# Performance work log

Measured on AMD Instinct MI355X. Metric: run time of the kernel, lower is better.

The kernel has to match this reference:

```python
import jax, jax.numpy as jnp
import numpy as np

N_NODES = 50000
N_EDGES = 800000
D = 64        # in_channels == out_channels
EDGE_DIM = 32
H = 8         # num_heads
HD = D // H   # head_dim


def _layer_norm(x, g, b, eps=1e-5):
    m = jnp.mean(x, axis=-1, keepdims=True)
    v = jnp.mean((x - m) ** 2, axis=-1, keepdims=True)
    return (x - m) * jax.lax.rsqrt(v + eps) * g + b


def setup_inputs() -> dict:
    key = jax.random.key(0)
    ks = jax.random.split(key, 20)
    s = 0.05
    inp = {
        'x': jax.random.normal(ks[0], (N_NODES, D), jnp.float32),
        'edge_index': jax.random.randint(ks[1], (2, N_EDGES), 0, N_NODES, dtype=jnp.int64),
        'edge_attr': jax.random.normal(ks[2], (N_EDGES, EDGE_DIM), jnp.float32),
        'Wq': jax.random.normal(ks[3], (D, D), jnp.float32) * s,
        'bq': jnp.zeros((D,), jnp.float32),
        'Wk': jax.random.normal(ks[4], (D, D), jnp.float32) * s,
        'bk': jnp.zeros((D,), jnp.float32),
        'Wv': jax.random.normal(ks[5], (D, D), jnp.float32) * s,
        'bv': jnp.zeros((D,), jnp.float32),
        'We': jax.random.normal(ks[6], (EDGE_DIM, D), jnp.float32) * s,
        'be': jnp.zeros((D,), jnp.float32),
        'Wo': jax.random.normal(ks[7], (D, D), jnp.float32) * s,
        'bo': jnp.zeros((D,), jnp.float32),
        'g1': jnp.ones((D,), jnp.float32),
        'b1': jnp.zeros((D,), jnp.float32),
        'g2': jnp.ones((D,), jnp.float32),
        'b2': jnp.zeros((D,), jnp.float32),
        'Wf1': jax.random.normal(ks[8], (D, 2 * D), jnp.float32) * s,
        'bf1': jnp.zeros((2 * D,), jnp.float32),
        'Wf2': jax.random.normal(ks[9], (2 * D, D), jnp.float32) * s,
        'bf2': jnp.zeros((D,), jnp.float32),
    }
    return inp


def reference(x, edge_index, edge_attr, Wq, bq, Wk, bk, Wv, bv, We, be, Wo, bo,
              g1, b1, g2, b2, Wf1, bf1, Wf2, bf2):
    num_nodes = x.shape[0]
    # add_self_loops with fill_value=0.0
    ar = jnp.arange(num_nodes, dtype=edge_index.dtype)
    src = jnp.concatenate([edge_index[0], ar])
    dst = jnp.concatenate([edge_index[1], ar])
    ea = jnp.concatenate([edge_attr, jnp.zeros((num_nodes, edge_attr.shape[1]), edge_attr.dtype)])

    q = (x @ Wq + bq).reshape(num_nodes, H, HD)
    k = (x @ Wk + bk).reshape(num_nodes, H, HD)
    v = (x @ Wv + bv).reshape(num_nodes, H, HD)
    ee = (ea @ We + be).reshape(-1, H, HD)  # [E', H, HD]

    # gather, score, global softmax over all edges (dim=0, as in source)
    scores = jnp.sum(q[dst] * (k[src] + ee), axis=-1) / (HD ** 0.5)  # [E', H]
    alpha = jax.nn.softmax(scores, axis=0)
    messages = alpha[..., None] * (v[src] + ee)  # [E', H, HD]

    out_sum = jax.ops.segment_sum(messages, dst, num_segments=num_nodes)
    counts = jax.ops.segment_sum(jnp.ones(dst.shape, x.dtype), dst, num_segments=num_nodes)
    counts = jnp.maximum(counts, 1.0)
    out = (out_sum / counts[:, None, None]).reshape(num_nodes, -1)

    h = _layer_norm(x + out @ Wo + bo, g1, b1)
    ffn = jax.nn.gelu(h @ Wf1 + bf1, approximate=False) @ Wf2 + bf2
    # dropout in eval mode -> identity
    return _layer_norm(h + ffn, g2, b2)
```

## Files before the change

### kernel.cpp

```cpp
#include <hip/hip_runtime.h>
#include <hip/hip_bf16.h>
#include <math.h>

#define N_NODES 50000
#define N_EDGES 800000
#define D 64
#define ED 32
#define NB 196

#define Q_OFF    0
#define KV8_OFF  1600000
#define EE_OFF   3200000
#define OS_OFF   16000000
#define S_OFF    17600000
#define RP_OFF   17600016
#define SRCP_OFF 17650018
#define POSE_OFF 18450018
#define DEG_OFF  19250018
#define WOFF_OFF 19300018
#define BSUM_OFF 19350018
#define H_OFF    0
#define F1_OFF   EE_OFF

typedef __bf16 bf16x8 __attribute__((ext_vector_type(8)));
typedef float  f32x4  __attribute__((ext_vector_type(4)));

__device__ __forceinline__ ushort f2bf(float f) {
  uint u = __float_as_uint(f);
  uint r = (u + 0x7FFFu + ((u >> 16) & 1u)) >> 16;
  return (ushort)r;
}
__device__ __forceinline__ float bfu2f(ushort u) {
  return __uint_as_float(((uint)u) << 16);
}
__device__ __forceinline__ void unpack8(uint4 u, float (&f)[8]) {
  f[0] = __uint_as_float(u.x << 16); f[1] = __uint_as_float(u.x & 0xffff0000u);
  f[2] = __uint_as_float(u.y << 16); f[3] = __uint_as_float(u.y & 0xffff0000u);
  f[4] = __uint_as_float(u.z << 16); f[5] = __uint_as_float(u.z & 0xffff0000u);
  f[6] = __uint_as_float(u.w << 16); f[7] = __uint_as_float(u.w & 0xffff0000u);
}
__device__ __forceinline__ void unfp8(uint2 u, float (&f)[8]) {
  f[0] = __builtin_amdgcn_cvt_f32_fp8((int)u.x, 0);
  f[1] = __builtin_amdgcn_cvt_f32_fp8((int)u.x, 1);
  f[2] = __builtin_amdgcn_cvt_f32_fp8((int)u.x, 2);
  f[3] = __builtin_amdgcn_cvt_f32_fp8((int)u.x, 3);
  f[4] = __builtin_amdgcn_cvt_f32_fp8((int)u.y, 0);
  f[5] = __builtin_amdgcn_cvt_f32_fp8((int)u.y, 1);
  f[6] = __builtin_amdgcn_cvt_f32_fp8((int)u.y, 2);
  f[7] = __builtin_amdgcn_cvt_f32_fp8((int)u.y, 3);
}
__device__ __forceinline__ bf16x8 pack_bf8(float4 a, float4 b) {
  bf16x8 r;
  r[0] = (__bf16)a.x; r[1] = (__bf16)a.y; r[2] = (__bf16)a.z; r[3] = (__bf16)a.w;
  r[4] = (__bf16)b.x; r[5] = (__bf16)b.y; r[6] = (__bf16)b.z; r[7] = (__bf16)b.w;
  return r;
}
__device__ __forceinline__ uint pk_fp8(f32x4 acc) {
  uint rr = (uint)__builtin_amdgcn_cvt_pk_fp8_f32(acc[0], acc[1], 0, false);
  return (uint)__builtin_amdgcn_cvt_pk_fp8_f32(acc[2], acc[3], (int)rr, true);
}

__global__ __launch_bounds__(256) void k_qkv_mfma(
    const float* __restrict__ x,
    const float* __restrict__ Wq, const float* __restrict__ bq,
    const float* __restrict__ Wk, const float* __restrict__ bk,
    const float* __restrict__ Wv, const float* __restrict__ bv,
    ushort* __restrict__ q, unsigned char* __restrict__ kv8,
    int* __restrict__ deg, float* __restrict__ S) {
  const int tid0 = blockIdx.x * 256 + threadIdx.x;
  if (tid0 < N_NODES) deg[tid0] = 0;
  if (tid0 < 16) S[tid0] = 0.f;

  const int lane = threadIdx.x & 63;
  const int wid  = threadIdx.x >> 6;
  const int r  = lane & 15;
  const int kg = lane >> 4;
  const float* Ws[3] = {Wq, Wk, Wv};
  const float* bs[3] = {bq, bk, bv};

  bf16x8 afrag[3][4][2];
  float  bias[3][4][4];
#pragma unroll
  for (int m = 0; m < 3; ++m)
#pragma unroll
    for (int nt = 0; nt < 4; ++nt) {
#pragma unroll
      for (int kk = 0; kk < 2; ++kk)
#pragma unroll
        for (int j = 0; j < 8; ++j)
          afrag[m][nt][kk][j] = (__bf16)Ws[m][(kk * 32 + kg * 8 + j) * 64 + nt * 16 + r];
#pragma unroll
      for (int j = 0; j < 4; ++j) bias[m][nt][j] = bs[m][nt * 16 + kg * 4 + j];
    }

  const int ntile = N_NODES / 16;
  const int nw = gridDim.x * 4;
  for (int t = blockIdx.x * 4 + wid; t < ntile; t += nw) {
    const int base = t * 16;
    const float4* xr = reinterpret_cast<const float4*>(x + (size_t)(base + r) * 64 + kg * 8);
    const bf16x8 xf0 = pack_bf8(xr[0], xr[1]);
    const bf16x8 xf1 = pack_bf8(xr[8], xr[9]);
#pragma unroll
    for (int m = 0; m < 3; ++m) {
#pragma unroll
      for (int nt = 0; nt < 4; ++nt) {
        f32x4 acc = {bias[m][nt][0], bias[m][nt][1], bias[m][nt][2], bias[m][nt][3]};
        acc = __builtin_amdgcn_mfma_f32_16x16x32_bf16(afrag[m][nt][0], xf0, acc, 0, 0, 0);
        acc = __builtin_amdgcn_mfma_f32_16x16x32_bf16(afrag[m][nt][1], xf1, acc, 0, 0, 0);
        if (m == 0) {
          ushort4 pk;
          pk.x = f2bf(acc[0]); pk.y = f2bf(acc[1]); pk.z = f2bf(acc[2]); pk.w = f2bf(acc[3]);
          *reinterpret_cast<ushort4*>(q + (size_t)(base + r) * 64 + nt * 16 + kg * 4) = pk;
        } else {
          const int sub = (m == 1) ? 0 : 8;
          const size_t off = (size_t)(base + r) * 128 +
                             (size_t)(nt * 2 + (kg >> 1)) * 16 + sub + (kg & 1) * 4;
          *reinterpret_cast<uint*>(kv8 + off) = pk_fp8(acc);
        }
      }
    }
  }
}

__global__ __launch_bounds__(256) void k_hist(const int* __restrict__ edst,
                                              int* __restrict__ deg) {
  const int i = blockIdx.x * 256 + threadIdx.x;
  if (i < N_EDGES) atomicAdd(&deg[edst[i]], 1);
}

__global__ __launch_bounds__(256) void k_scan_a(const int* __restrict__ deg,
                                                int* __restrict__ bsum) {
  __shared__ int lds[256];
  const int i = blockIdx.x * 256 + threadIdx.x;
  lds[threadIdx.x] = (i < N_NODES) ? deg[i] : 0;
  __syncthreads();
  for (int s = 128; s > 0; s >>= 1) {
    if (threadIdx.x < s) lds[threadIdx.x] += lds[threadIdx.x + s];
    __syncthreads();
  }
  if (threadIdx.x == 0) bsum[blockIdx.x] = lds[0];
}

__global__ __launch_bounds__(256) void k_scan_c(const int* __restrict__ deg,
                                                const int* __restrict__ bsum,
                                                int* __restrict__ rowptr,
                                                int* __restrict__ woff) {
  __shared__ int lds[256];
  const int t = threadIdx.x;
  lds[t] = (t < blockIdx.x) ? bsum[t] : 0;
  __syncthreads();
  for (int s = 128; s > 0; s >>= 1) {
    if (t < s) lds[t] += lds[t + s];
    __syncthreads();
  }
  const int base0 = lds[0];
  __syncthreads();
  const int i = blockIdx.x * 256 + t;
  const int d = (i < N_NODES) ? deg[i] : 0;
  lds[t] = d;
  __syncthreads();
  for (int off = 1; off < 256; off <<= 1) {
    const int val = (t >= off) ? lds[t - off] : 0;
    __syncthreads();
    lds[t] += val;
    __syncthreads();
  }
  const int ex = base0 + lds[t] - d;
  if (i < N_NODES) { rowptr[i] = ex; woff[i] = ex; }
  if (i == N_NODES - 1) rowptr[N_NODES] = ex + d;
}

__global__ __launch_bounds__(256) void k_scatter(const int* __restrict__ esrc,
                                                 const int* __restrict__ edst,
                                                 int* __restrict__ woff,
                                                 int* __restrict__ srcp,
                                                 int* __restrict__ pose) {
  const int i = blockIdx.x * 256 + threadIdx.x;
  if (i < N_EDGES) {
    const int pos = atomicAdd(&woff[edst[i]], 1);
    srcp[pos] = esrc[i];
    pose[i] = pos;
  }
}

__global__ __launch_bounds__(256) void k_ee_mfma(
    const int* __restrict__ pose, const float* __restrict__ ea,
    const float* __restrict__ We, const float* __restrict__ be,
    unsigned char* __restrict__ ee8) {
  const int lane = threadIdx.x & 63;
  const int wid  = threadIdx.x >> 6;
  const int r  = lane & 15;
  const int kg = lane >> 4;

  bf16x8 afrag[4];
  float  bias[4][4];
#pragma unroll
  for (int nt = 0; nt < 4; ++nt) {
#pragma unroll
    for (int j = 0; j < 8; ++j)
      afrag[nt][j] = (__bf16)We[(kg * 8 + j) * 64 + nt * 16 + r];
#pragma unroll
    for (int j = 0; j < 4; ++j) bias[nt][j] = be[nt * 16 + kg * 4 + j];
  }

  const int ntile = N_EDGES / 16;
  const int nw = gridDim.x * 4;
  for (int t = blockIdx.x * 4 + wid; t < ntile; t += nw) {
    const int base = t * 16;
    const int pos = pose[base + r];
    const float4* ar = reinterpret_cast<const float4*>(ea + (size_t)(base + r) * 32 + kg * 8);
    const bf16x8 bfrag = pack_bf8(ar[0], ar[1]);
#pragma unroll
    for (int nt = 0; nt < 4; ++nt) {
      f32x4 acc = {bias[nt][0], bias[nt][1], bias[nt][2], bias[nt][3]};
      acc = __builtin_amdgcn_mfma_f32_16x16x32_bf16(afrag[nt], bfrag, acc, 0, 0, 0);
      *reinterpret_cast<uint*>(ee8 + (size_t)pos * 64 + nt * 16 + kg * 4) = pk_fp8(acc);
    }
  }
}

__global__ __launch_bounds__(256) void k_gather(
    const int* __restrict__ rowptr, const int* __restrict__ srcp,
    const unsigned char* __restrict__ ee8,
    const ushort* __restrict__ qb, const unsigned char* __restrict__ kv8,
    const float* __restrict__ be,
    ushort* __restrict__ osum, float* __restrict__ S) {
  const int lane = threadIdx.x & 63;
  const int wid  = threadIdx.x >> 6;
  const int h = lane & 7, ei = lane >> 3;
  float bes[8];
#pragma unroll
  for (int i = 0; i < 8; ++i) bes[i] = be[h * 8 + i];
  float sacc = 0.f;
  const int nw = gridDim.x * 4;
  for (int n = blockIdx.x * 4 + wid; n < N_NODES; n += nw) {
    const int beg = rowptr[n], end = rowptr[n + 1];
    float qv[8];
    unpack8(*reinterpret_cast<const uint4*>(qb + (size_t)n * 64 + h * 8), qv);
    float macc[8];
#pragma unroll
    for (int i = 0; i < 8; ++i) macc[i] = 0.f;
    if (ei == 0) {
      float kv[8], vv[8];
      const uint4 kvl = *reinterpret_cast<const uint4*>(kv8 + (size_t)n * 128 + h * 16);
      unfp8(make_uint2(kvl.x, kvl.y), kv);
      unfp8(make_uint2(kvl.z, kvl.w), vv);
      float sc = 0.f;
#pragma unroll
      for (int i = 0; i < 8; ++i) sc = fmaf(qv[i], kv[i] + bes[i], sc);
      const float w = __expf(sc * 0.3535533905932738f);
      sacc += w;
#pragma unroll
      for (int i = 0; i < 8; ++i) macc[i] = w * (vv[i] + bes[i]);
    }
    int p = beg + ei;
    int src = (p < end) ? srcp[p] : 0;
    for (; p < end; p += 8) {
      const int nsrc = (p + 8 < end) ? srcp[p + 8] : 0;
      float ev[8], kv[8], vv[8];
      unfp8(*reinterpret_cast<const uint2*>(ee8 + (size_t)p * 64 + h * 8), ev);
      const uint4 kvl = *reinterpret_cast<const uint4*>(kv8 + (size_t)src * 128 + h * 16);
      unfp8(make_uint2(kvl.x, kvl.y), kv);
      unfp8(make_uint2(kvl.z, kvl.w), vv);
      float sc = 0.f;
#pragma unroll
      for (int i = 0; i < 8; ++i) sc = fmaf(qv[i], kv[i] + ev[i], sc);
      const float w = __expf(sc * 0.3535533905932738f);
      sacc += w;
#pragma unroll
      for (int i = 0; i < 8; ++i) macc[i] = fmaf(w, vv[i] + ev[i], macc[i]);
      src = nsrc;
    }
#pragma unroll
    for (int i = 0; i < 8; ++i) {
      macc[i] += __shfl_xor(macc[i], 8);
      macc[i] += __shfl_xor(macc[i], 16);
      macc[i] += __shfl_xor(macc[i], 32);
    }
    if (ei == 0) {
      uint pk[4];
#pragma unroll
      for (int i = 0; i < 4; ++i)
        pk[i] = (uint)f2bf(macc[2 * i]) | ((uint)f2bf(macc[2 * i + 1]) << 16);
      *reinterpret_cast<uint4*>(osum + (size_t)n * 64 + h * 8) =
          make_uint4(pk[0], pk[1], pk[2], pk[3]);
    }
  }
  sacc += __shfl_xor(sacc, 8);
  sacc += __shfl_xor(sacc, 16);
  sacc += __shfl_xor(sacc, 32);
  if (ei == 0) atomicAdd(&S[h], sacc);
}

__global__ __launch_bounds__(256) void k_ln1_mfma(
    const ushort* __restrict__ osum, const int* __restrict__ rowptr,
    const float* __restrict__ S, const float* __restrict__ x,
    const float* __restrict__ Wo, const float* __restrict__ bo,
    const float* __restrict__ g1, const float* __restrict__ b1,
    ushort* __restrict__ h) {
  const int lane = threadIdx.x & 63;
  const int wid  = threadIdx.x >> 6;
  const int r  = lane & 15;
  const int kg = lane >> 4;

  bf16x8 afrag[4][2];
  float bias[4][4], g1f[4][4], b1f[4][4];
#pragma unroll
  for (int nt = 0; nt < 4; ++nt) {
#pragma unroll
    for (int kk = 0; kk < 2; ++kk)
#pragma unroll
      for (int j = 0; j < 8; ++j)
        afrag[nt][kk][j] = (__bf16)Wo[(kk * 32 + kg * 8 + j) * 64 + nt * 16 + r];
#pragma unroll
    for (int j = 0; j < 4; ++j) {
      bias[nt][j] = bo[nt * 16 + kg * 4 + j];
      g1f[nt][j]  = g1[nt * 16 + kg * 4 + j];
      b1f[nt][j]  = b1[nt * 16 + kg * 4 + j];
    }
  }
  float invSv[8];
#pragma unroll
  for (int i = 0; i < 8; ++i) invSv[i] = 1.0f / S[i];

  const int ntile = N_NODES / 16;
  const int nw = gridDim.x * 4;
  for (int t = blockIdx.x * 4 + wid; t < ntile; t += nw) {
    const int node = t * 16 + r;
    const float invc = 1.0f / (float)(rowptr[node + 1] - rowptr[node] + 1);
    bf16x8 bfrag[2];
#pragma unroll
    for (int kk = 0; kk < 2; ++kk) {
      float tmp[8];
      unpack8(*reinterpret_cast<const uint4*>(osum + (size_t)node * 64 + kk * 32 + kg * 8), tmp);
      const float sc = invSv[kk * 4 + kg] * invc;
      bf16x8 bf;
#pragma unroll
      for (int e = 0; e < 8; ++e) bf[e] = (__bf16)(tmp[e] * sc);
      bfrag[kk] = bf;
    }
    float tv[4][4];
    float sum = 0.f;
#pragma unroll
    for (int nt = 0; nt < 4; ++nt) {
      f32x4 acc = {bias[nt][0], bias[nt][1], bias[nt][2], bias[nt][3]};
      acc = __builtin_amdgcn_mfma_f32_16x16x32_bf16(afrag[nt][0], bfrag[0], acc, 0, 0, 0);
      acc = __builtin_amdgcn_mfma_f32_16x16x32_bf16(afrag[nt][1], bfrag[1], acc, 0, 0, 0);
      const float4 xv = *reinterpret_cast<const float4*>(x + (size_t)node * 64 + nt * 16 + kg * 4);
      tv[nt][0] = acc[0] + xv.x; tv[nt][1] = acc[1] + xv.y;
      tv[nt][2] = acc[2] + xv.z; tv[nt][3] = acc[3] + xv.w;
      sum += (tv[nt][0] + tv[nt][1]) + (tv[nt][2] + tv[nt][3]);
    }
    sum += __shfl_xor(sum, 16);
    sum += __shfl_xor(sum, 32);
    const float m = sum * (1.0f / 64.0f);
    float var = 0.f;
#pragma unroll
    for (int nt = 0; nt < 4; ++nt)
#pragma unroll
      for (int j = 0; j < 4; ++j) { const float d = tv[nt][j] - m; var = fmaf(d, d, var); }
    var += __shfl_xor(var, 16);
    var += __shfl_xor(var, 32);
    const float rinv = rsqrtf(var * (1.0f / 64.0f) + 1e-5f);
#pragma unroll
    for (int nt = 0; nt < 4; ++nt) {
      ushort4 pk;
      pk.x = f2bf((tv[nt][0] - m) * rinv * g1f[nt][0] + b1f[nt][0]);
      pk.y = f2bf((tv[nt][1] - m) * rinv * g1f[nt][1] + b1f[nt][1]);
      pk.z = f2bf((tv[nt][2] - m) * rinv * g1f[nt][2] + b1f[nt][2]);
      pk.w = f2bf((tv[nt][3] - m) * rinv * g1f[nt][3] + b1f[nt][3]);
      *reinterpret_cast<ushort4*>(h + (size_t)node * 64 + nt * 16 + kg * 4) = pk;
    }
  }
}

__global__ __launch_bounds__(256) void k_ffn1_mfma(
    const ushort* __restrict__ h, const float* __restrict__ Wf1,
    const float* __restrict__ bf1, ushort* __restrict__ f1) {
  const int lane = threadIdx.x & 63;
  const int wid  = threadIdx.x >> 6;
  const int r  = lane & 15;
  const int kg = lane >> 4;

  bf16x8 afrag[8][2];
  float bias[8][4];
#pragma unroll
  for (int nt = 0; nt < 8; ++nt) {
#pragma unroll
    for (int kk = 0; kk < 2; ++kk)
#pragma unroll
      for (int j = 0; j < 8; ++j)
        afrag[nt][kk][j] = (__bf16)Wf1[(kk * 32 + kg * 8 + j) * 128 + nt * 16 + r];
#pragma unroll
    for (int j = 0; j < 4; ++j) bias[nt][j] = bf1[nt * 16 + kg * 4 + j];
  }

  const int ntile = N_NODES / 16;
  const int nw = gridDim.x * 4;
  for (int t = blockIdx.x * 4 + wid; t < ntile; t += nw) {
    const int node = t * 16 + r;
    const bf16x8 bf0 = *reinterpret_cast<const bf16x8*>(h + (size_t)node * 64 + kg * 8);
    const bf16x8 bf1g = *reinterpret_cast<const bf16x8*>(h + (size_t)node * 64 + 32 + kg * 8);
#pragma unroll
    for (int nt = 0; nt < 8; ++nt) {
      f32x4 acc = {bias[nt][0], bias[nt][1], bias[nt][2], bias[nt][3]};
      acc = __builtin_amdgcn_mfma_f32_16x16x32_bf16(afrag[nt][0], bf0, acc, 0, 0, 0);
      acc = __builtin_amdgcn_mfma_f32_16x16x32_bf16(afrag[nt][1], bf1g, acc, 0, 0, 0);
      ushort4 pk;
      pk.x = f2bf(0.5f * acc[0] * (1.0f + erff(acc[0] * 0.7071067811865475f)));
      pk.y = f2bf(0.5f * acc[1] * (1.0f + erff(acc[1] * 0.7071067811865475f)));
      pk.z = f2bf(0.5f * acc[2] * (1.0f + erff(acc[2] * 0.7071067811865475f)));
      pk.w = f2bf(0.5f * acc[3] * (1.0f + erff(acc[3] * 0.7071067811865475f)));
      *reinterpret_cast<ushort4*>(f1 + (size_t)node * 128 + nt * 16 + kg * 4) = pk;
    }
  }
}

__global__ __launch_bounds__(256) void k_ffn2_mfma(
    const ushort* __restrict__ f1, const ushort* __restrict__ h,
    const float* __restrict__ Wf2, const float* __restrict__ bf2,
    const float* __restrict__ g2, const float* __restrict__ b2,
    float* __restrict__ out) {
  const int lane = threadIdx.x & 63;
  const int wid  = threadIdx.x >> 6;
  const int r  = lane & 15;
  const int kg = lane >> 4;

  bf16x8 afrag[4][4];
  float bias[4][4], g2f[4][4], b2f[4][4];
#pragma unroll
  for (int nt = 0; nt < 4; ++nt) {
#pragma unroll
    for (int kk = 0; kk < 4; ++kk)
#pragma unroll
      for (int j = 0; j < 8; ++j)
        afrag[nt][kk][j] = (__bf16)Wf2[(kk * 32 + kg * 8 + j) * 64 + nt * 16 + r];
#pragma unroll
    for (int j = 0; j < 4; ++j) {
      bias[nt][j] = bf2[nt * 16 + kg * 4 + j];
      g2f[nt][j]  = g2[nt * 16 + kg * 4 + j];
      b2f[nt][j]  = b2[nt * 16 + kg * 4 + j];
    }
  }

  const int ntile = N_NODES / 16;
  const int nw = gridDim.x * 4;
  for (int t = blockIdx.x * 4 + wid; t < ntile; t += nw) {
    const int node = t * 16 + r;
    bf16x8 bfrag[4];
#pragma unroll
    for (int kk = 0; kk < 4; ++kk)
      bfrag[kk] = *reinterpret_cast<const bf16x8*>(f1 + (size_t)node * 128 + kk * 32 + kg * 8);
    float tv[4][4];
    float sum = 0.f;
#pragma unroll
    for (int nt = 0; nt < 4; ++nt) {
      f32x4 acc = {bias[nt][0], bias[nt][1], bias[nt][2], bias[nt][3]};
      acc = __builtin_amdgcn_mfma_f32_16x16x32_bf16(afrag[nt][0], bfrag[0], acc, 0, 0, 0);
      acc = __builtin_amdgcn_mfma_f32_16x16x32_bf16(afrag[nt][1], bfrag[1], acc, 0, 0, 0);
      acc = __builtin_amdgcn_mfma_f32_16x16x32_bf16(afrag[nt][2], bfrag[2], acc, 0, 0, 0);
      acc = __builtin_amdgcn_mfma_f32_16x16x32_bf16(afrag[nt][3], bfrag[3], acc, 0, 0, 0);
      const ushort4 hv = *reinterpret_cast<const ushort4*>(h + (size_t)node * 64 + nt * 16 + kg * 4);
      tv[nt][0] = acc[0] + bfu2f(hv.x); tv[nt][1] = acc[1] + bfu2f(hv.y);
      tv[nt][2] = acc[2] + bfu2f(hv.z); tv[nt][3] = acc[3] + bfu2f(hv.w);
      sum += (tv[nt][0] + tv[nt][1]) + (tv[nt][2] + tv[nt][3]);
    }
    sum += __shfl_xor(sum, 16);
    sum += __shfl_xor(sum, 32);
    const float m = sum * (1.0f / 64.0f);
    float var = 0.f;
#pragma unroll
    for (int nt = 0; nt < 4; ++nt)
#pragma unroll
      for (int j = 0; j < 4; ++j) { const float d = tv[nt][j] - m; var = fmaf(d, d, var); }
    var += __shfl_xor(var, 16);
    var += __shfl_xor(var, 32);
    const float rinv = rsqrtf(var * (1.0f / 64.0f) + 1e-5f);
#pragma unroll
    for (int nt = 0; nt < 4; ++nt) {
      float4 o;
      o.x = (tv[nt][0] - m) * rinv * g2f[nt][0] + b2f[nt][0];
      o.y = (tv[nt][1] - m) * rinv * g2f[nt][1] + b2f[nt][1];
      o.z = (tv[nt][2] - m) * rinv * g2f[nt][2] + b2f[nt][2];
      o.w = (tv[nt][3] - m) * rinv * g2f[nt][3] + b2f[nt][3];
      *reinterpret_cast<float4*>(out + (size_t)node * 64 + nt * 16 + kg * 4) = o;
    }
  }
}

extern "C" void kernel_launch(void* const* d_in, const int* in_sizes, int n_in,
                              void* d_out, int out_size, void* d_ws, size_t ws_size,
                              hipStream_t stream) {
  const float* x    = (const float*)d_in[0];
  const int*   ei   = (const int*)d_in[1];
  const int*   esrc = ei;
  const int*   edst = ei + N_EDGES;
  const float* ea   = (const float*)d_in[2];
  const float* Wq   = (const float*)d_in[3];
  const float* bq   = (const float*)d_in[4];
  const float* Wk   = (const float*)d_in[5];
  const float* bk   = (const float*)d_in[6];
  const float* Wv   = (const float*)d_in[7];
  const float* bv   = (const float*)d_in[8];
  const float* We   = (const float*)d_in[9];
  const float* be   = (const float*)d_in[10];
  const float* Wo   = (const float*)d_in[11];
  const float* bo   = (const float*)d_in[12];
  const float* g1   = (const float*)d_in[13];
  const float* b1   = (const float*)d_in[14];
  const float* g2   = (const float*)d_in[15];
  const float* b2   = (const float*)d_in[16];
  const float* Wf1  = (const float*)d_in[17];
  const float* bf1  = (const float*)d_in[18];
  const float* Wf2  = (const float*)d_in[19];
  const float* bf2  = (const float*)d_in[20];

  float* ws    = (float*)d_ws;
  ushort* q    = (ushort*)(ws + Q_OFF);
  unsigned char* kv8 = (unsigned char*)(ws + KV8_OFF);
  unsigned char* ee8 = (unsigned char*)(ws + EE_OFF);
  ushort* osum = (ushort*)(ws + OS_OFF);
  float* S     = ws + S_OFF;
  int*   rowptr = (int*)(ws + RP_OFF);
  int*   srcp   = (int*)(ws + SRCP_OFF);
  int*   pose   = (int*)(ws + POSE_OFF);
  int*   deg    = (int*)(ws + DEG_OFF);
  int*   woff   = (int*)(ws + WOFF_OFF);
  int*   bsum   = (int*)(ws + BSUM_OFF);
  ushort* h    = (ushort*)(ws + H_OFF);
  ushort* f1   = (ushort*)(ws + F1_OFF);
  float* out   = (float*)d_out;

  const dim3 B(256);
  const int edgeBlocks = (N_EDGES + 255) / 256;

  k_qkv_mfma<<<dim3(256), B, 0, stream>>>(x, Wq, bq, Wk, bk, Wv, bv, q, kv8, deg, S);
  k_hist<<<dim3(edgeBlocks), B, 0, stream>>>(edst, deg);
  k_scan_a<<<dim3(NB), B, 0, stream>>>(deg, bsum);
  k_scan_c<<<dim3(NB), B, 0, stream>>>(deg, bsum, rowptr, woff);
  k_scatter<<<dim3(edgeBlocks), B, 0, stream>>>(esrc, edst, woff, srcp, pose);
  k_ee_mfma<<<dim3(1024), B, 0, stream>>>(pose, ea, We, be, ee8);
  k_gather<<<dim3(1024), B, 0, stream>>>(rowptr, srcp, ee8, q, kv8, be, osum, S);
  k_ln1_mfma<<<dim3(256), B, 0, stream>>>(osum, rowptr, S, x, Wo, bo, g1, b1, h);
  k_ffn1_mfma<<<dim3(256), B, 0, stream>>>(h, Wf1, bf1, f1);
  k_ffn2_mfma<<<dim3(256), B, 0, stream>>>(f1, h, Wf2, bf2, g2, b2, out);
}
```

Measured before the change: 268.0 us.

## Fuse LN1, FFN1 and FFN2 into one post-attention kernel via LDS staging

Measured after the change: 264.2 us (median of 2 runs). About the same (-1.4%).

```diff
diff --git a/kernel.cpp b/kernel.cpp
--- a/kernel.cpp
+++ b/kernel.cpp
@@ -19,8 +19,6 @@
 #define DEG_OFF  19250018
 #define WOFF_OFF 19300018
 #define BSUM_OFF 19350018
-#define H_OFF    0
-#define F1_OFF   EE_OFF
 
 typedef __bf16 bf16x8 __attribute__((ext_vector_type(8)));
 typedef float  f32x4  __attribute__((ext_vector_type(4)));
@@ -292,32 +290,59 @@
   if (ei == 0) atomicAdd(&S[h], sacc);
 }
 
-__global__ __launch_bounds__(256) void k_ln1_mfma(
+#define HST 72
+#define FST 136
+__global__ __launch_bounds__(256, 1) void k_post(
     const ushort* __restrict__ osum, const int* __restrict__ rowptr,
     const float* __restrict__ S, const float* __restrict__ x,
     const float* __restrict__ Wo, const float* __restrict__ bo,
     const float* __restrict__ g1, const float* __restrict__ b1,
-    ushort* __restrict__ h) {
+    const float* __restrict__ Wf1, const float* __restrict__ bf1,
+    const float* __restrict__ Wf2, const float* __restrict__ bf2,
+    const float* __restrict__ g2, const float* __restrict__ b2,
+    float* __restrict__ out) {
+  __shared__ ushort hls[4][16 * HST];
+  __shared__ ushort f1ls[4][16 * FST];
   const int lane = threadIdx.x & 63;
   const int wid  = threadIdx.x >> 6;
   const int r  = lane & 15;
   const int kg = lane >> 4;
-
-  bf16x8 afrag[4][2];
-  float bias[4][4], g1f[4][4], b1f[4][4];
+  ushort* hbase  = &hls[wid][0];
+  ushort* f1base = &f1ls[wid][0];
+
+  bf16x8 wo[4][2], w1[8][2], w2[4][4];
+  float bof[4][4], g1f[4][4], b1f[4][4], b1v[8][4], bf2f[4][4], g2f[4][4], b2f[4][4];
 #pragma unroll
   for (int nt = 0; nt < 4; ++nt) {
 #pragma unroll
     for (int kk = 0; kk < 2; ++kk)
 #pragma unroll
       for (int j = 0; j < 8; ++j)
-        afrag[nt][kk][j] = (__bf16)Wo[(kk * 32 + kg * 8 + j) * 64 + nt * 16 + r];
+        wo[nt][kk][j] = (__bf16)Wo[(kk * 32 + kg * 8 + j) * 64 + nt * 16 + r];
+#pragma unroll
+    for (int kk = 0; kk < 4; ++kk)
+#pragma unroll
+      for (int j = 0; j < 8; ++j)
+        w2[nt][kk][j] = (__bf16)Wf2[(kk * 32 + kg * 8 + j) * 64 + nt * 16 + r];
 #pragma unroll
     for (int j = 0; j < 4; ++j) {
-      bias[nt][j] = bo[nt * 16 + kg * 4 + j];
-      g1f[nt][j]  = g1[nt * 16 + kg * 4 + j];
-      b1f[nt][j]  = b1[nt * 16 + kg * 4 + j];
-    }
+      bof[nt][j] = bo[nt * 16 + kg * 4 + j];
+      g1f[nt][j] = g1[nt * 16 + kg * 4 + j];
+      b1f[nt][j] = b1[nt * 16 + kg * 4 + j];
+      bf2f[nt][j] = bf2[nt * 16 + kg * 4 + j];
+      g2f[nt][j] = g2[nt * 16 + kg * 4 + j];
+      b2f[nt][j] = b2[nt * 16 + kg * 4 + j];
+    }
+  }
+#pragma unroll
+  for (int nt = 0; nt < 8; ++nt) {
+#pragma unroll
+    for (int kk = 0; kk < 2; ++kk)
+#pragma unroll
+      for (int j = 0; j < 8; ++j)
+        w1[nt][kk][j] = (__bf16)Wf1[(kk * 32 + kg * 8 + j) * 128 + nt * 16 + r];
+#pragma unroll
+    for (int j = 0; j < 4; ++j) b1v[nt][j] = bf1[nt * 16 + kg * 4 + j];
   }
   float invSv[8];
 #pragma unroll
@@ -343,9 +368,9 @@
     float sum = 0.f;
 #pragma unroll
     for (int nt = 0; nt < 4; ++nt) {
-      f32x4 acc = {bias[nt][0], bias[nt][1], bias[nt][2], bias[nt][3]};
-      acc = __builtin_amdgcn_mfma_f32_16x16x32_bf16(afrag[nt][0], bfrag[0], acc, 0, 0, 0);
-      acc = __builtin_amdgcn_mfma_f32_16x16x32_bf16(afrag[nt][1], bfrag[1], acc, 0, 0, 0);
+      f32x4 acc = {bof[nt][0], bof[nt][1], bof[nt][2], bof[nt][3]};
+      acc = __builtin_amdgcn_mfma_f32_16x16x32_bf16(wo[nt][0], bfrag[0], acc, 0, 0, 0);
+      acc = __builtin_amdgcn_mfma_f32_16x16x32_bf16(wo[nt][1], bfrag[1], acc, 0, 0, 0);
       const float4 xv = *reinterpret_cast<const float4*>(x + (size_t)node * 64 + nt * 16 + kg * 4);
       tv[nt][0] = acc[0] + xv.x; tv[nt][1] = acc[1] + xv.y;
       tv[nt][2] = acc[2] + xv.z; tv[nt][3] = acc[3] + xv.w;
@@ -362,127 +387,67 @@
     var += __shfl_xor(var, 16);
     var += __shfl_xor(var, 32);
     const float rinv = rsqrtf(var * (1.0f / 64.0f) + 1e-5f);
+    float hn[4][4];
 #pragma unroll
     for (int nt = 0; nt < 4; ++nt) {
+#pragma unroll
+      for (int j = 0; j < 4; ++j)
+        hn[nt][j] = (tv[nt][j] - m) * rinv * g1f[nt][j] + b1f[nt][j];
       ushort4 pk;
-      pk.x = f2bf((tv[nt][0] - m) * rinv * g1f[nt][0] + b1f[nt][0]);
-      pk.y = f2bf((tv[nt][1] - m) * rinv * g1f[nt][1] + b1f[nt][1]);
-      pk.z = f2bf((tv[nt][2] - m) * rinv * g1f[nt][2] + b1f[nt][2]);
-      pk.w = f2bf((tv[nt][3] - m) * rinv * g1f[nt][3] + b1f[nt][3]);
-      *reinterpret_cast<ushort4*>(h + (size_t)node * 64 + nt * 16 + kg * 4) = pk;
-    }
-  }
-}
-
-__global__ __launch_bounds__(256) void k_ffn1_mfma(
-    const ushort* __restrict__ h, const float* __restrict__ Wf1,
-    const float* __restrict__ bf1, ushort* __restrict__ f1) {
-  const int lane = threadIdx.x & 63;
-  const int wid  = threadIdx.x >> 6;
-  const int r  = lane & 15;
-  const int kg = lane >> 4;
-
-  bf16x8 afrag[8][2];
-  float bias[8][4];
-#pragma unroll
-  for (int nt = 0; nt < 8; ++nt) {
+      pk.x = f2bf(hn[nt][0]); pk.y = f2bf(hn[nt][1]);
+      pk.z = f2bf(hn[nt][2]); pk.w = f2bf(hn[nt][3]);
+      *reinterpret_cast<ushort4*>(hbase + r * HST + nt * 16 + kg * 4) = pk;
+    }
+    bf16x8 hB[2];
 #pragma unroll
     for (int kk = 0; kk < 2; ++kk)
-#pragma unroll
-      for (int j = 0; j < 8; ++j)
-        afrag[nt][kk][j] = (__bf16)Wf1[(kk * 32 + kg * 8 + j) * 128 + nt * 16 + r];
-#pragma unroll
-    for (int j = 0; j < 4; ++j) bias[nt][j] = bf1[nt * 16 + kg * 4 + j];
-  }
-
-  const int ntile = N_NODES / 16;
-  const int nw = gridDim.x * 4;
-  for (int t = blockIdx.x * 4 + wid; t < ntile; t += nw) {
-    const int node = t * 16 + r;
-    const bf16x8 bf0 = *reinterpret_cast<const bf16x8*>(h + (size_t)node * 64 + kg * 8);
-    const bf16x8 bf1g = *reinterpret_cast<const bf16x8*>(h + (size_t)node * 64 + 32 + kg * 8);
+      hB[kk] = *reinterpret_cast<const bf16x8*>(hbase + r * HST + kk * 32 + kg * 8);
 #pragma unroll
     for (int nt = 0; nt < 8; ++nt) {
-      f32x4 acc = {bias[nt][0], bias[nt][1], bias[nt][2], bias[nt][3]};
-      acc = __builtin_amdgcn_mfma_f32_16x16x32_bf16(afrag[nt][0], bf0, acc, 0, 0, 0);
-      acc = __builtin_amdgcn_mfma_f32_16x16x32_bf16(afrag[nt][1], bf1g, acc, 0, 0, 0);
+      f32x4 acc = {b1v[nt][0], b1v[nt][1], b1v[nt][2], b1v[nt][3]};
+      acc = __builtin_amdgcn_mfma_f32_16x16x32_bf16(w1[nt][0], hB[0], acc, 0, 0, 0);
+      acc = __builtin_amdgcn_mfma_f32_16x16x32_bf16(w1[nt][1], hB[1], acc, 0, 0, 0);
       ushort4 pk;
       pk.x = f2bf(0.5f * acc[0] * (1.0f + erff(acc[0] * 0.7071067811865475f)));
       pk.y = f2bf(0.5f * acc[1] * (1.0f + erff(acc[1] * 0.7071067811865475f)));
       pk.z = f2bf(0.5f * acc[2] * (1.0f + erff(acc[2] * 0.7071067811865475f)));
       pk.w = f2bf(0.5f * acc[3] * (1.0f + erff(acc[3] * 0.7071067811865475f)));
-      *reinterpret_cast<ushort4*>(f1 + (size_t)node * 128 + nt * 16 + kg * 4) = pk;
-    }
-  }
-}
-
-__global__ __launch_bounds__(256) void k_ffn2_mfma(
-    const ushort* __restrict__ f1, const ushort* __restrict__ h,
-    const float* __restrict__ Wf2, const float* __restrict__ bf2,
-    const float* __restrict__ g2, const float* __restrict__ b2,
-    float* __restrict__ out) {
-  const int lane = threadIdx.x & 63;
-  const int wid  = threadIdx.x >> 6;
-  const int r  = lane & 15;
-  const int kg = lane >> 4;
-
-  bf16x8 afrag[4][4];
-  float bias[4][4], g2f[4][4], b2f[4][4];
-#pragma unroll
-  for (int nt = 0; nt < 4; ++nt) {
+      *reinterpret_cast<ushort4*>(f1base + r * FST + nt * 16 + kg * 4) = pk;
+    }
+    bf16x8 fB[4];
 #pragma unroll
     for (int kk = 0; kk < 4; ++kk)
-#pragma unroll
-      for (int j = 0; j < 8; ++j)
-        afrag[nt][kk][j] = (__bf16)Wf2[(kk * 32 + kg * 8 + j) * 64 + nt * 16 + r];
-#pragma unroll
-    for (int j = 0; j < 4; ++j) {
-      bias[nt][j] = bf2[nt * 16 + kg * 4 + j];
-      g2f[nt][j]  = g2[nt * 16 + kg * 4 + j];
-      b2f[nt][j]  = b2[nt * 16 + kg * 4 + j];
-    }
-  }
-
-  const int ntile = N_NODES / 16;
-  const int nw = gridDim.x * 4;
-  for (int t = blockIdx.x * 4 + wid; t < ntile; t += nw) {
-    const int node = t * 16 + r;
-    bf16x8 bfrag[4];
-#pragma unroll
-    for (int kk = 0; kk < 4; ++kk)
-      bfrag[kk] = *reinterpret_cast<const bf16x8*>(f1 + (size_t)node * 128 + kk * 32 + kg * 8);
-    float tv[4][4];
-    float sum = 0.f;
+      fB[kk] = *reinterpret_cast<const bf16x8*>(f1base + r * FST + kk * 32 + kg * 8);
+    float sum2 = 0.f;
 #pragma unroll
     for (int nt = 0; nt < 4; ++nt) {
-      f32x4 acc = {bias[nt][0], bias[nt][1], bias[nt][2], bias[nt][3]};
-      acc = __builtin_amdgcn_mfma_f32_16x16x32_bf16(afrag[nt][0], bfrag[0], acc, 0, 0, 0);
-      acc = __builtin_amdgcn_mfma_f32_16x16x32_bf16(afrag[nt][1], bfrag[1], acc, 0, 0, 0);
-      acc = __builtin_amdgcn_mfma_f32_16x16x32_bf16(afrag[nt][2], bfrag[2], acc, 0, 0, 0);
-      acc = __builtin_amdgcn_mfma_f32_16x16x32_bf16(afrag[nt][3], bfrag[3], acc, 0, 0, 0);
-      const ushort4 hv = *reinterpret_cast<const ushort4*>(h + (size_t)node * 64 + nt * 16 + kg * 4);
-      tv[nt][0] = acc[0] + bfu2f(hv.x); tv[nt][1] = acc[1] + bfu2f(hv.y);
-      tv[nt][2] = acc[2] + bfu2f(hv.z); tv[nt][3] = acc[3] + bfu2f(hv.w);
-      sum += (tv[nt][0] + tv[nt][1]) + (tv[nt][2] + tv[nt][3]);
-    }
-    sum += __shfl_xor(sum, 16);
-    sum += __shfl_xor(sum, 32);
-    const float m = sum * (1.0f / 64.0f);
-    float var = 0.f;
+      f32x4 acc = {bf2f[nt][0], bf2f[nt][1], bf2f[nt][2], bf2f[nt][3]};
+      acc = __builtin_amdgcn_mfma_f32_16x16x32_bf16(w2[nt][0], fB[0], acc, 0, 0, 0);
+      acc = __builtin_amdgcn_mfma_f32_16x16x32_bf16(w2[nt][1], fB[1], acc, 0, 0, 0);
+      acc = __builtin_amdgcn_mfma_f32_16x16x32_bf16(w2[nt][2], fB[2], acc, 0, 0, 0);
+      acc = __builtin_amdgcn_mfma_f32_16x16x32_bf16(w2[nt][3], fB[3], acc, 0, 0, 0);
+      tv[nt][0] = acc[0] + hn[nt][0]; tv[nt][1] = acc[1] + hn[nt][1];
+      tv[nt][2] = acc[2] + hn[nt][2]; tv[nt][3] = acc[3] + hn[nt][3];
+      sum2 += (tv[nt][0] + tv[nt][1]) + (tv[nt][2] + tv[nt][3]);
+    }
+    sum2 += __shfl_xor(sum2, 16);
+    sum2 += __shfl_xor(sum2, 32);
+    const float m2 = sum2 * (1.0f / 64.0f);
+    float var2 = 0.f;
 #pragma unroll
     for (int nt = 0; nt < 4; ++nt)
 #pragma unroll
-      for (int j = 0; j < 4; ++j) { const float d = tv[nt][j] - m; var = fmaf(d, d, var); }
-    var += __shfl_xor(var, 16);
-    var += __shfl_xor(var, 32);
-    const float rinv = rsqrtf(var * (1.0f / 64.0f) + 1e-5f);
+      for (int j = 0; j < 4; ++j) { const float d = tv[nt][j] - m2; var2 = fmaf(d, d, var2); }
+    var2 += __shfl_xor(var2, 16);
+    var2 += __shfl_xor(var2, 32);
+    const float rinv2 = rsqrtf(var2 * (1.0f / 64.0f) + 1e-5f);
 #pragma unroll
     for (int nt = 0; nt < 4; ++nt) {
       float4 o;
-      o.x = (tv[nt][0] - m) * rinv * g2f[nt][0] + b2f[nt][0];
-      o.y = (tv[nt][1] - m) * rinv * g2f[nt][1] + b2f[nt][1];
-      o.z = (tv[nt][2] - m) * rinv * g2f[nt][2] + b2f[nt][2];
-      o.w = (tv[nt][3] - m) * rinv * g2f[nt][3] + b2f[nt][3];
+      o.x = (tv[nt][0] - m2) * rinv2 * g2f[nt][0] + b2f[nt][0];
+      o.y = (tv[nt][1] - m2) * rinv2 * g2f[nt][1] + b2f[nt][1];
+      o.z = (tv[nt][2] - m2) * rinv2 * g2f[nt][2] + b2f[nt][2];
+      o.w = (tv[nt][3] - m2) * rinv2 * g2f[nt][3] + b2f[nt][3];
       *reinterpret_cast<float4*>(out + (size_t)node * 64 + nt * 16 + kg * 4) = o;
     }
   }
@@ -527,8 +492,6 @@
   int*   deg    = (int*)(ws + DEG_OFF);
   int*   woff   = (int*)(ws + WOFF_OFF);
   int*   bsum   = (int*)(ws + BSUM_OFF);
-  ushort* h    = (ushort*)(ws + H_OFF);
-  ushort* f1   = (ushort*)(ws + F1_OFF);
   float* out   = (float*)d_out;
 
   const dim3 B(256);
@@ -541,7 +504,6 @@
   k_scatter<<<dim3(edgeBlocks), B, 0, stream>>>(esrc, edst, woff, srcp, pose);
   k_ee_mfma<<<dim3(1024), B, 0, stream>>>(pose, ea, We, be, ee8);
   k_gather<<<dim3(1024), B, 0, stream>>>(rowptr, srcp, ee8, q, kv8, be, osum, S);
-  k_ln1_mfma<<<dim3(256), B, 0, stream>>>(osum, rowptr, S, x, Wo, bo, g1, b1, h);
-  k_ffn1_mfma<<<dim3(256), B, 0, stream>>>(h, Wf1, bf1, f1);
-  k_ffn2_mfma<<<dim3(256), B, 0, stream>>>(f1, h, Wf2, bf2, g2, b2, out);
-}
+  k_post<<<dim3(256), B, 0, stream>>>(osum, rowptr, S, x, Wo, bo, g1, b1,
+                                      Wf1, bf1, Wf2, bf2, g2, b2, out);
+}
```
